# Kernel tuning notes

Hardware: AMD Instinct MI355X
Metric: run time of the kernel (lower is better)

Reference implementation:

```python
import jax, jax.numpy as jnp
import numpy as np
import math

B, S, HID, H = 1, 2048, 1024, 16
D = HID // H  # head_dim = 64


def setup_inputs() -> dict:
    key = jax.random.key(0)
    ks = jax.random.split(key, 12)
    s = 0.02
    x = jax.random.normal(ks[0], (B, S, HID), jnp.float32)
    Wq = jax.random.normal(ks[1], (HID, HID), jnp.float32) * s
    bq = jnp.zeros((HID,), jnp.float32)
    Wk = jax.random.normal(ks[2], (HID, HID), jnp.float32) * s
    bk = jnp.zeros((HID,), jnp.float32)
    Wv = jax.random.normal(ks[3], (HID, HID), jnp.float32) * s
    bv = jnp.zeros((HID,), jnp.float32)
    Wo = jax.random.normal(ks[4], (HID, HID), jnp.float32) * s
    bo = jnp.zeros((HID,), jnp.float32)
    # nn.Parameter(torch.ones(3,3)) at init; small noise so the bias is non-degenerate
    cmw = jnp.ones((3, 3), jnp.float32) + 0.1 * jax.random.normal(ks[5], (3, 3), jnp.float32)
    # full causal [B,S,S] mask so the mask.shape[1]==seq_len branch is taken
    mask = jnp.tril(jnp.ones((B, S, S), jnp.int32))
    modality_info = jax.random.randint(ks[6], (B, S), 0, 3, dtype=jnp.int64)
    return dict(x=x, Wq=Wq, bq=bq, Wk=Wk, bk=bk, Wv=Wv, bv=bv, Wo=Wo, bo=bo,
                cmw=cmw, mask=mask, modality_info=modality_info)


def reference(x, Wq, bq, Wk, bk, Wv, bv, Wo, bo, cmw, mask, modality_info):
    b, s, _ = x.shape
    # QKV projections (torch Linear: y = x @ W.T + b), split into heads [B,H,S,D]
    q = (x @ Wq.T + bq).reshape(b, s, H, D).transpose(0, 2, 1, 3)
    k = (x @ Wk.T + bk).reshape(b, s, H, D).transpose(0, 2, 1, 3)
    v = (x @ Wv.T + bv).reshape(b, s, H, D).transpose(0, 2, 1, 3)
    scores = jnp.einsum('bhqd,bhkd->bhqk', q, k) / math.sqrt(D)  # [B,H,S,S]
    # cross-modal bias: gather from 3x3 table via pairwise modality indices -> [B,S,S]
    bias = cmw[modality_info[:, :, None], modality_info[:, None, :]]
    scores = scores + bias[:, None, :, :]  # equals original broadcast when B==1
    scores = jnp.where(mask[:, None, :, :] == 0, -1e9, scores)
    attn = jax.nn.softmax(scores, axis=-1)  # dropout is identity in eval
    ctx = jnp.einsum('bhqk,bhkd->bhqd', attn, v)          # [B,H,S,D]
    ctx = ctx.transpose(0, 2, 1, 3).reshape(b, s, HID)    # [B,S,HID]
    return ctx @ Wo.T + bo
```

## Files before the change

kernel.cpp:

```cpp
#include <hip/hip_runtime.h>
#include <hip/hip_bf16.h>
#include <math.h>

#define S_LEN 2048
#define HID   1024
#define NHEAD 16

using bf16x8 = __attribute__((ext_vector_type(8))) short;
using bf16x4 = __attribute__((ext_vector_type(4))) short;
using f32x4  = __attribute__((ext_vector_type(4))) float;

__device__ __forceinline__ float bf2f(short s) {
  union { unsigned u; float f; } c;
  c.u = ((unsigned)(unsigned short)s) << 16;
  return c.f;
}
__device__ __forceinline__ short f2bf(float f) {
  union { float f; unsigned u; } c; c.f = f;
  unsigned u = c.u;
  unsigned r = (u + 0x7fffu + ((u >> 16) & 1u)) >> 16;
  return (short)r;
}
__device__ __forceinline__ float loadf(const void* base, long idx, int is_bf) {
  return is_bf ? bf2f(((const short*)base)[idx]) : ((const float*)base)[idx];
}
__device__ __forceinline__ void gl_lds16(const void* g, void* l) {
  __builtin_amdgcn_global_load_lds(
      (const __attribute__((address_space(1))) void*)g,
      (__attribute__((address_space(3))) void*)l, 16, 0, 0);
}

__global__ void detect_kernel(const unsigned* __restrict__ xw,
                              const int* __restrict__ modw,
                              int* __restrict__ flags) {
  const int t = threadIdx.x;
  int cnt = 0;
  for (int i = t; i < 1024; i += 64) {
    const unsigned fld = (xw[i] >> 7) & 0xFFu;
    cnt += (fld >= 100u && fld <= 135u) ? 1 : 0;
  }
  int odd = 0;
  for (int i = 0; i < 4; ++i) {
    const int wv = modw[2 * (t + 64 * i) + 1];
    odd += (wv != 0) ? 1 : 0;
  }
  for (int m = 1; m < 64; m <<= 1) {
    cnt += __shfl_xor(cnt, m);
    odd += __shfl_xor(odd, m);
  }
  if (t == 0) {
    flags[0] = (cnt >= 512) ? 1 : 0;
    flags[1] = (odd == 0) ? 1 : 0;
  }
}

__global__ __launch_bounds__(256) void convert5(
    const void* __restrict__ s0, const void* __restrict__ s1, const void* __restrict__ s2,
    const void* __restrict__ s3, const void* __restrict__ s4,
    short* __restrict__ d0, short* __restrict__ d1, short* __restrict__ d2,
    short* __restrict__ d3, short* __restrict__ d4,
    const int* __restrict__ flags) {
  const int a = blockIdx.y;
  const void* src = (a == 0) ? s0 : (a == 1) ? s1 : (a == 2) ? s2 : (a == 3) ? s3 : s4;
  short* dst = (a == 0) ? d0 : (a == 1) ? d1 : (a == 2) ? d2 : (a == 3) ? d3 : d4;
  const long n = (a == 0) ? (2L << 20) : (1L << 20);
  const int is_bf = flags[0];
  long i = (long)(blockIdx.x * 256 + threadIdx.x) * 8;
  const long stride = (long)gridDim.x * 256 * 8;
  if (is_bf) {
    for (; i < n; i += stride)
      *(bf16x8*)(dst + i) = *(const bf16x8*)((const short*)src + i);
  } else {
    for (; i < n; i += stride) {
      const float* p = (const float*)src + i;
      bf16x8 r;
#pragma unroll
      for (int j = 0; j < 8; ++j) r[j] = f2bf(p[j]);
      *(bf16x8*)(dst + i) = r;
    }
  }
}

__global__ __launch_bounds__(256) void gemm_bt3(
    const short* __restrict__ A,
    const short* __restrict__ W0, const short* __restrict__ W1, const short* __restrict__ W2,
    const void* __restrict__ b0, const void* __restrict__ b1, const void* __restrict__ b2,
    void* __restrict__ C0, void* __restrict__ C1, void* __restrict__ C2,
    const int* __restrict__ flags, int nbn, int store_f32)
{
  constexpr int K = 1024;
  constexpr int N = 1024;
  __shared__ short As[128 * 32];
  __shared__ short Bs[64 * 32];

  const int t = threadIdx.x;
  const int w = t >> 6, lane = t & 63;
  const int l15 = lane & 15, quad = lane >> 4;
  const int wm = w >> 1, wn = w & 1;
  const int is_bf = flags[0];

  const int mat = blockIdx.x / nbn;
  const int n0 = (blockIdx.x % nbn) * 64;
  const int m0 = blockIdx.y * 128;

  const short* W  = (mat == 0) ? W0 : (mat == 1 ? W1 : W2);
  const void* bia = (mat == 0) ? b0 : (mat == 1 ? b1 : b2);
  void*       C   = (mat == 0) ? C0 : (mat == 1 ? C1 : C2);

  f32x4 acc[4][2];
  for (int mi = 0; mi < 4; ++mi)
    for (int ni = 0; ni < 2; ++ni)
      for (int r = 0; r < 4; ++r) acc[mi][ni][r] = 0.f;

  const int srow = t >> 2;
  const int sch  = (t & 3) * 8;
  const short* Ap = A + (long)(m0 + srow) * K + sch;
  const short* Wp = W + (long)(n0 + srow) * K + sch;
  short* AsW = &As[w * 512];
  short* BsW = &Bs[w * 512];

  for (int kt = 0; kt < K / 32; ++kt) {
    __syncthreads();
    gl_lds16(Ap + kt * 32, AsW);
    gl_lds16(Ap + kt * 32 + 64L * K, AsW + 2048);
    gl_lds16(Wp + kt * 32, BsW);
    __syncthreads();

    bf16x8 af[4], bfr[2];
    for (int mi = 0; mi < 4; ++mi)
      af[mi] = *(const bf16x8*)&As[(wm * 64 + mi * 16 + l15) * 32 + quad * 8];
    for (int ni = 0; ni < 2; ++ni)
      bfr[ni] = *(const bf16x8*)&Bs[(wn * 32 + ni * 16 + l15) * 32 + quad * 8];
    for (int mi = 0; mi < 4; ++mi)
      for (int ni = 0; ni < 2; ++ni)
        acc[mi][ni] = __builtin_amdgcn_mfma_f32_16x16x32_bf16(af[mi], bfr[ni], acc[mi][ni], 0, 0, 0);
  }

  for (int ni = 0; ni < 2; ++ni) {
    const int col = n0 + wn * 32 + ni * 16 + l15;
    const float bv = loadf(bia, col, is_bf);
    for (int mi = 0; mi < 4; ++mi) {
      const int row = m0 + wm * 64 + mi * 16 + quad * 4;
      for (int r = 0; r < 4; ++r) {
        const float v = acc[mi][ni][r] + bv;
        const long idx = (long)(row + r) * N + col;
        if (store_f32) ((float*)C)[idx] = v;
        else           ((short*)C)[idx] = f2bf(v);
      }
    }
  }
}

__global__ __launch_bounds__(256) void attn_split(
    const short* __restrict__ Q, const short* __restrict__ Kg, const short* __restrict__ Vg,
    const int* __restrict__ mod, const void* __restrict__ cmw,
    const int* __restrict__ flags,
    short* __restrict__ PO0, short* __restrict__ PO1,
    float* __restrict__ PL)
{
  __shared__ short Ks[64 * 80];
  __shared__ short Vt[64 * 80];
  __shared__ short Ps[4 * 16 * 80];
  __shared__ float cm[9];
  __shared__ int mods[2048];

  const int t = threadIdx.x;
  const int w = t >> 6, lane = t & 63;
  const int l15 = lane & 15, quad = lane >> 4;
  const int h = blockIdx.y;
  const int pair = blockIdx.x >> 1;
  const int par  = blockIdx.x & 1;
  const int m64 = flags[1];

  if (t < 9) cm[t] = loadf(cmw, t, flags[0]);
  for (int i = t; i < 2048; i += 256) mods[i] = mod[i << m64];
  __syncthreads();

  short* POp = (par == 0) ? PO0 : PO1;
  const int krow = t >> 3, kch = (t & 7) * 8;
  const int vkp = t & 63, vdc = (t >> 6) * 8;

  for (int si = 0; si < 2; ++si) {
    const int strip = (si == 0) ? pair : 31 - pair;
    const int q0 = strip * 64;
    const int nkt = strip + 1;

    const short* qb = Q + (long)(q0 + w * 16 + l15) * HID + h * 64 + quad * 8;
    const bf16x8 aq0 = *(const bf16x8*)qb;
    const bf16x8 aq1 = *(const bf16x8*)(qb + 32);

    int mrow[4];
    for (int r = 0; r < 4; ++r) mrow[r] = mods[q0 + w * 16 + quad * 4 + r];

    float lsum[4];
    f32x4 acc_o[4];
    for (int r = 0; r < 4; ++r) lsum[r] = 0.f;
    for (int ni = 0; ni < 4; ++ni)
      for (int r = 0; r < 4; ++r) acc_o[ni][r] = 0.f;

    bf16x8 rk0, rk1, rv0, rv1;
    if (par < nkt) {
      const long kb = (long)(par * 64) * HID + h * 64;
      rk0 = *(const bf16x8*)(Kg + kb + (long)krow * HID + kch);
      rk1 = *(const bf16x8*)(Kg + kb + (long)(krow + 32) * HID + kch);
      rv0 = *(const bf16x8*)(Vg + kb + (long)vkp * HID + vdc);
      rv1 = *(const bf16x8*)(Vg + kb + (long)vkp * HID + 32 + vdc);
    }

    for (int kt = par; kt < nkt; kt += 2) {
      __syncthreads();
      *(bf16x8*)&Ks[krow * 80 + kch] = rk0;
      *(bf16x8*)&Ks[(krow + 32) * 80 + kch] = rk1;
#pragma unroll
      for (int j = 0; j < 8; ++j) Vt[(vdc + j) * 80 + vkp] = rv0[j];
#pragma unroll
      for (int j = 0; j < 8; ++j) Vt[(vdc + 32 + j) * 80 + vkp] = rv1[j];
      __syncthreads();
      if (kt + 2 < nkt) {
        const long kb = (long)((kt + 2) * 64) * HID + h * 64;
        rk0 = *(const bf16x8*)(Kg + kb + (long)krow * HID + kch);
        rk1 = *(const bf16x8*)(Kg + kb + (long)(krow + 32) * HID + kch);
        rv0 = *(const bf16x8*)(Vg + kb + (long)vkp * HID + vdc);
        rv1 = *(const bf16x8*)(Vg + kb + (long)vkp * HID + 32 + vdc);
      }

      f32x4 sc[4];
      for (int nt = 0; nt < 4; ++nt) {
        const bf16x8 kb0 = *(const bf16x8*)&Ks[(nt * 16 + l15) * 80 + quad * 8];
        const bf16x8 kb1 = *(const bf16x8*)&Ks[(nt * 16 + l15) * 80 + 32 + quad * 8];
        f32x4 z;
        for (int r = 0; r < 4; ++r) z[r] = 0.f;
        z = __builtin_amdgcn_mfma_f32_16x16x32_bf16(aq0, kb0, z, 0, 0, 0);
        z = __builtin_amdgcn_mfma_f32_16x16x32_bf16(aq1, kb1, z, 0, 0, 0);
        sc[nt] = z;
      }

      float sv[4][4];
      for (int nt = 0; nt < 4; ++nt) {
        const int mcol = mods[kt * 64 + nt * 16 + l15];
        for (int r = 0; r < 4; ++r)
          sv[nt][r] = sc[nt][r] * 0.125f + cm[mrow[r] * 3 + mcol];
      }
      if (kt == nkt - 1) {
        for (int nt = 0; nt < 4; ++nt) {
          const int col = kt * 64 + nt * 16 + l15;
          for (int r = 0; r < 4; ++r) {
            const int row = q0 + w * 16 + quad * 4 + r;
            sv[nt][r] = (col <= row) ? sv[nt][r] : -1e30f;
          }
        }
      }
      short pb[4][4];
      for (int nt = 0; nt < 4; ++nt)
        for (int r = 0; r < 4; ++r) {
          const float p = __expf(fminf(sv[nt][r], 60.f));
          lsum[r] += p;
          pb[nt][r] = f2bf(p);
        }

      short* Pw = &Ps[w * 16 * 80];
      for (int nt = 0; nt < 4; ++nt)
        for (int r = 0; r < 4; ++r)
          Pw[(quad * 4 + r) * 80 + nt * 16 + l15] = pb[nt][r];
      asm volatile("s_waitcnt lgkmcnt(0)" ::: "memory");

      for (int kk = 0; kk < 2; ++kk) {
        const bf16x8 ap = *(const bf16x8*)&Pw[l15 * 80 + kk * 32 + quad * 8];
        for (int ni = 0; ni < 4; ++ni) {
          const bf16x8 bv = *(const bf16x8*)&Vt[(ni * 16 + l15) * 80 + kk * 32 + quad * 8];
          acc_o[ni] = __builtin_amdgcn_mfma_f32_16x16x32_bf16(ap, bv, acc_o[ni], 0, 0, 0);
        }
      }
    }

    for (int off = 1; off < 16; off <<= 1)
      for (int r = 0; r < 4; ++r) lsum[r] += __shfl_xor(lsum[r], off);

    for (int ni = 0; ni < 4; ++ni) {
      const int col = h * 64 + ni * 16 + l15;
      for (int r = 0; r < 4; ++r) {
        const int row = q0 + w * 16 + quad * 4 + r;
        POp[(long)row * HID + col] = f2bf(acc_o[ni][r]);
      }
    }
    if (l15 == 0) {
      for (int r = 0; r < 4; ++r) {
        const int row = q0 + w * 16 + quad * 4 + r;
        PL[par * 32768 + row * 16 + h] = lsum[r];
      }
    }
  }
}

__global__ __launch_bounds__(256) void attn_merge(
    const short* __restrict__ PO0, const short* __restrict__ PO1,
    const float* __restrict__ PL, short* __restrict__ CTX)
{
  const int row = blockIdx.x;
  const int t = threadIdx.x;
  const int h = t >> 4;
  const int d0 = (t & 15) * 4;
  const float l0 = PL[row * 16 + h], l1 = PL[32768 + row * 16 + h];
  const float inv = 1.f / (l0 + l1);
  const long b = (long)row * HID + h * 64 + d0;
  const bf16x4 o0 = *(const bf16x4*)&PO0[b];
  const bf16x4 o1 = *(const bf16x4*)&PO1[b];
  bf16x4 out;
#pragma unroll
  for (int j = 0; j < 4; ++j)
    out[j] = f2bf((bf2f(o0[j]) + bf2f(o1[j])) * inv);
  *(bf16x4*)&CTX[b] = out;
}

extern "C" void kernel_launch(void* const* d_in, const int* in_sizes, int n_in,
                              void* d_out, int out_size, void* d_ws, size_t ws_size,
                              hipStream_t stream) {
  constexpr long M1 = 1024L * 1024L;
  int*   flags = (int*)d_ws;
  short* base  = (short*)d_ws + 128;
  short* xb  = base;
  short* Wqb = xb + 2 * M1;
  short* Wkb = Wqb + M1;
  short* Wvb = Wkb + M1;
  short* Wob = Wvb + M1;
  short* Qw  = Wob + M1;
  short* Kw  = Qw + 2 * M1;
  short* Vw  = Kw + 2 * M1;
  short* CTX = Vw + 2 * M1;
  short* PO0 = CTX;
  short* PO1 = xb;
  float* PL  = (float*)Wvb;
  const int* modality = (const int*)d_in[11];

  detect_kernel<<<1, 64, 0, stream>>>((const unsigned*)d_in[0], modality, flags);
  convert5<<<dim3(512, 5), 256, 0, stream>>>(
      d_in[0], d_in[1], d_in[3], d_in[5], d_in[7],
      xb, Wqb, Wkb, Wvb, Wob, flags);

  gemm_bt3<<<dim3(48, 16), 256, 0, stream>>>(
      xb, Wqb, Wkb, Wvb, d_in[2], d_in[4], d_in[6],
      Qw, Kw, Vw, flags, 16, 0);
  attn_split<<<dim3(32, NHEAD), 256, 0, stream>>>(
      Qw, Kw, Vw, modality, d_in[9], flags, PO0, PO1, PL);
  attn_merge<<<dim3(S_LEN), 256, 0, stream>>>(PO0, PO1, PL, CTX);
  gemm_bt3<<<dim3(16, 16), 256, 0, stream>>>(
      CTX, Wob, Wob, Wob, d_in[8], d_in[8], d_in[8],
      d_out, d_out, d_out, flags, 16, 1);
}
```

Baseline: 183.2 us.

## Fuse attention split-merge into output projection GEMM and use K=64 steps

Removes the separate attn_merge kernel. The output-projection GEMM now reads both partial attention outputs and their row sums, normalizes them in registers, and writes the merged A tile into LDS. It also changes both GEMMs to load two 32-wide K slices per barrier pair, which halves the number of syncs. The cost is extra global traffic inside the O-proj GEMM, because each column block re-reads PO0/PO1 and recomputes the merge, and LDS use is larger.

```diff
diff --git a/kernel.cpp b/kernel.cpp
--- a/kernel.cpp
+++ b/kernel.cpp
@@ -7,7 +7,6 @@
 #define NHEAD 16
 
 using bf16x8 = __attribute__((ext_vector_type(8))) short;
-using bf16x4 = __attribute__((ext_vector_type(4))) short;
 using f32x4  = __attribute__((ext_vector_type(4))) float;
 
 __device__ __forceinline__ float bf2f(short s) {
@@ -90,8 +89,8 @@
 {
   constexpr int K = 1024;
   constexpr int N = 1024;
-  __shared__ short As[128 * 32];
-  __shared__ short Bs[64 * 32];
+  __shared__ short As[2][128 * 32];
+  __shared__ short Bs[2][64 * 32];
 
   const int t = threadIdx.x;
   const int w = t >> 6, lane = t & 63;
@@ -116,24 +115,33 @@
   const int sch  = (t & 3) * 8;
   const short* Ap = A + (long)(m0 + srow) * K + sch;
   const short* Wp = W + (long)(n0 + srow) * K + sch;
-  short* AsW = &As[w * 512];
-  short* BsW = &Bs[w * 512];
-
-  for (int kt = 0; kt < K / 32; ++kt) {
+  short* AsW0 = &As[0][w * 512];
+  short* AsW1 = &As[1][w * 512];
+  short* BsW0 = &Bs[0][w * 512];
+  short* BsW1 = &Bs[1][w * 512];
+
+  for (int kt = 0; kt < K / 64; ++kt) {
+    const long kb = (long)kt * 64;
     __syncthreads();
-    gl_lds16(Ap + kt * 32, AsW);
-    gl_lds16(Ap + kt * 32 + 64L * K, AsW + 2048);
-    gl_lds16(Wp + kt * 32, BsW);
+    gl_lds16(Ap + kb, AsW0);
+    gl_lds16(Ap + kb + 64L * K, AsW0 + 2048);
+    gl_lds16(Wp + kb, BsW0);
+    gl_lds16(Ap + kb + 32, AsW1);
+    gl_lds16(Ap + kb + 32 + 64L * K, AsW1 + 2048);
+    gl_lds16(Wp + kb + 32, BsW1);
     __syncthreads();
 
-    bf16x8 af[4], bfr[2];
-    for (int mi = 0; mi < 4; ++mi)
-      af[mi] = *(const bf16x8*)&As[(wm * 64 + mi * 16 + l15) * 32 + quad * 8];
-    for (int ni = 0; ni < 2; ++ni)
-      bfr[ni] = *(const bf16x8*)&Bs[(wn * 32 + ni * 16 + l15) * 32 + quad * 8];
-    for (int mi = 0; mi < 4; ++mi)
+#pragma unroll
+    for (int s = 0; s < 2; ++s) {
+      bf16x8 af[4], bfr[2];
+      for (int mi = 0; mi < 4; ++mi)
+        af[mi] = *(const bf16x8*)&As[s][(wm * 64 + mi * 16 + l15) * 32 + quad * 8];
       for (int ni = 0; ni < 2; ++ni)
-        acc[mi][ni] = __builtin_amdgcn_mfma_f32_16x16x32_bf16(af[mi], bfr[ni], acc[mi][ni], 0, 0, 0);
+        bfr[ni] = *(const bf16x8*)&Bs[s][(wn * 32 + ni * 16 + l15) * 32 + quad * 8];
+      for (int mi = 0; mi < 4; ++mi)
+        for (int ni = 0; ni < 2; ++ni)
+          acc[mi][ni] = __builtin_amdgcn_mfma_f32_16x16x32_bf16(af[mi], bfr[ni], acc[mi][ni], 0, 0, 0);
+    }
   }
 
   for (int ni = 0; ni < 2; ++ni) {
@@ -292,24 +300,88 @@
   }
 }
 
-__global__ __launch_bounds__(256) void attn_merge(
+__global__ __launch_bounds__(256) void gemm_omerge(
     const short* __restrict__ PO0, const short* __restrict__ PO1,
-    const float* __restrict__ PL, short* __restrict__ CTX)
+    const float* __restrict__ PL,
+    const short* __restrict__ W, const void* __restrict__ bia,
+    float* __restrict__ C, const int* __restrict__ flags)
 {
-  const int row = blockIdx.x;
+  constexpr int K = 1024;
+  constexpr int N = 1024;
+  __shared__ short As[2][128 * 32];
+  __shared__ short Bs[2][64 * 32];
+
   const int t = threadIdx.x;
-  const int h = t >> 4;
-  const int d0 = (t & 15) * 4;
-  const float l0 = PL[row * 16 + h], l1 = PL[32768 + row * 16 + h];
-  const float inv = 1.f / (l0 + l1);
-  const long b = (long)row * HID + h * 64 + d0;
-  const bf16x4 o0 = *(const bf16x4*)&PO0[b];
-  const bf16x4 o1 = *(const bf16x4*)&PO1[b];
-  bf16x4 out;
-#pragma unroll
-  for (int j = 0; j < 4; ++j)
-    out[j] = f2bf((bf2f(o0[j]) + bf2f(o1[j])) * inv);
-  *(bf16x4*)&CTX[b] = out;
+  const int w = t >> 6, lane = t & 63;
+  const int l15 = lane & 15, quad = lane >> 4;
+  const int wm = w >> 1, wn = w & 1;
+  const int is_bf = flags[0];
+
+  const int n0 = blockIdx.x * 64;
+  const int m0 = blockIdx.y * 128;
+
+  f32x4 acc[4][2];
+  for (int mi = 0; mi < 4; ++mi)
+    for (int ni = 0; ni < 2; ++ni)
+      for (int r = 0; r < 4; ++r) acc[mi][ni][r] = 0.f;
+
+  const int srow = t >> 2;
+  const int sch  = (t & 3) * 8;
+  const long a0 = (long)(m0 + srow) * K + sch;
+  const long a1 = (long)(m0 + srow + 64) * K + sch;
+  const short* Wp = W + (long)(n0 + srow) * K + sch;
+  short* BsW0 = &Bs[0][w * 512];
+  short* BsW1 = &Bs[1][w * 512];
+
+  for (int kt = 0; kt < K / 64; ++kt) {
+    const long kb = (long)kt * 64;
+    const float inv0 = 1.f / (PL[(m0 + srow) * 16 + kt] + PL[32768 + (m0 + srow) * 16 + kt]);
+    const float inv1 = 1.f / (PL[(m0 + srow + 64) * 16 + kt] + PL[32768 + (m0 + srow + 64) * 16 + kt]);
+    bf16x8 mr[2][2];
+#pragma unroll
+    for (int s = 0; s < 2; ++s) {
+      const bf16x8 p00 = *(const bf16x8*)(PO0 + a0 + kb + s * 32);
+      const bf16x8 p01 = *(const bf16x8*)(PO1 + a0 + kb + s * 32);
+      const bf16x8 p10 = *(const bf16x8*)(PO0 + a1 + kb + s * 32);
+      const bf16x8 p11 = *(const bf16x8*)(PO1 + a1 + kb + s * 32);
+#pragma unroll
+      for (int j = 0; j < 8; ++j) {
+        mr[s][0][j] = f2bf((bf2f(p00[j]) + bf2f(p01[j])) * inv0);
+        mr[s][1][j] = f2bf((bf2f(p10[j]) + bf2f(p11[j])) * inv1);
+      }
+    }
+    __syncthreads();
+#pragma unroll
+    for (int s = 0; s < 2; ++s) {
+      *(bf16x8*)&As[s][srow * 32 + sch] = mr[s][0];
+      *(bf16x8*)&As[s][(srow + 64) * 32 + sch] = mr[s][1];
+    }
+    gl_lds16(Wp + kb, BsW0);
+    gl_lds16(Wp + kb + 32, BsW1);
+    __syncthreads();
+
+#pragma unroll
+    for (int s = 0; s < 2; ++s) {
+      bf16x8 af[4], bfr[2];
+      for (int mi = 0; mi < 4; ++mi)
+        af[mi] = *(const bf16x8*)&As[s][(wm * 64 + mi * 16 + l15) * 32 + quad * 8];
+      for (int ni = 0; ni < 2; ++ni)
+        bfr[ni] = *(const bf16x8*)&Bs[s][(wn * 32 + ni * 16 + l15) * 32 + quad * 8];
+      for (int mi = 0; mi < 4; ++mi)
+        for (int ni = 0; ni < 2; ++ni)
+          acc[mi][ni] = __builtin_amdgcn_mfma_f32_16x16x32_bf16(af[mi], bfr[ni], acc[mi][ni], 0, 0, 0);
+    }
+  }
+
+  for (int ni = 0; ni < 2; ++ni) {
+    const int col = n0 + wn * 32 + ni * 16 + l15;
+    const float bv = loadf(bia, col, is_bf);
+    for (int mi = 0; mi < 4; ++mi) {
+      const int row = m0 + wm * 64 + mi * 16 + quad * 4;
+      for (int r = 0; r < 4; ++r)
+        C[(long)(row + r) * N + col] = acc[mi][ni][r] + bv;
+    }
+  }
 }
 
 extern "C" void kernel_launch(void* const* d_in, const int* in_sizes, int n_in,
@@ -326,8 +398,7 @@
   short* Qw  = Wob + M1;
   short* Kw  = Qw + 2 * M1;
   short* Vw  = Kw + 2 * M1;
-  short* CTX = Vw + 2 * M1;
-  short* PO0 = CTX;
+  short* PO0 = Vw + 2 * M1;
   short* PO1 = xb;
   float* PL  = (float*)Wvb;
   const int* modality = (const int*)d_in[11];
@@ -342,8 +413,6 @@
       Qw, Kw, Vw, flags, 16, 0);
   attn_split<<<dim3(32, NHEAD), 256, 0, stream>>>(
       Qw, Kw, Vw, modality, d_in[9], flags, PO0, PO1, PL);
-  attn_merge<<<dim3(S_LEN), 256, 0, stream>>>(PO0, PO1, PL, CTX);
-  gemm_bt3<<<dim3(16, 16), 256, 0, stream>>>(
-      CTX, Wob, Wob, Wob, d_in[8], d_in[8], d_in[8],
-      d_out, d_out, d_out, flags, 16, 1);
-}
+  gemm_omerge<<<dim3(16, 16), 256, 0, stream>>>(
+      PO0, PO1, PL, Wob, d_in[8], (float*)d_out, flags);
+}
```

Measured after the change: 188.4 us. 2.8% more time.
